# Optimization experiments

Measured on AMD Instinct MI355X. Metric: run time of the kernel, lower is better.

## Reference

```python
import jax, jax.numpy as jnp
import numpy as np

N_NODES = 50000
N_EDGES = 500000
HIDDEN = 128
OUT = 64


def _sage_conv(x, edge_index, Wl, Wr, b):
    # PyG SAGEConv (aggr='mean', root_weight=True):
    # out_i = Wl @ mean_{j->i} x_j + Wr @ x_i + b
    src, dst = edge_index[0], edge_index[1]
    msgs = x[src]                                         # [E, d] gather
    summed = jax.ops.segment_sum(msgs, dst, num_segments=N_NODES)   # [N, d]
    deg = jax.ops.segment_sum(jnp.ones((msgs.shape[0],), x.dtype), dst,
                              num_segments=N_NODES)       # [N]
    agg = summed / jnp.maximum(deg, 1.0)[:, None]         # mean (0 if no in-edges)
    return agg @ Wl + x @ Wr + b


def setup_inputs() -> dict:
    key = jax.random.key(0)
    ks = jax.random.split(key, 11)
    s = 1.0 / np.sqrt(HIDDEN)
    inp = {
        "x": jax.random.normal(ks[0], (N_NODES, HIDDEN), jnp.float32),
        "edge_index": jax.random.randint(ks[1], (2, N_EDGES), 0, N_NODES, jnp.int32),
        "W1l": jax.random.normal(ks[2], (HIDDEN, HIDDEN), jnp.float32) * s,
        "W1r": jax.random.normal(ks[3], (HIDDEN, HIDDEN), jnp.float32) * s,
        "b1": jax.random.normal(ks[4], (HIDDEN,), jnp.float32) * s,
        "W2l": jax.random.normal(ks[5], (HIDDEN, HIDDEN), jnp.float32) * s,
        "W2r": jax.random.normal(ks[6], (HIDDEN, HIDDEN), jnp.float32) * s,
        "b2": jax.random.normal(ks[7], (HIDDEN,), jnp.float32) * s,
        "W3l": jax.random.normal(ks[8], (HIDDEN, OUT), jnp.float32) * s,
        "W3r": jax.random.normal(ks[9], (HIDDEN, OUT), jnp.float32) * s,
        "b3": jax.random.normal(ks[10], (OUT,), jnp.float32) * s,
    }
    return inp


def reference(x, edge_index, W1l, W1r, b1, W2l, W2r, b2, W3l, W3r, b3):
    h = jax.nn.relu(_sage_conv(x, edge_index, W1l, W1r, b1))
    h = jax.nn.relu(_sage_conv(h, edge_index, W2l, W2r, b2))
    return _sage_conv(h, edge_index, W3l, W3r, b3)
```

## Files before the change

### kernel.cpp

```cpp
#include <hip/hip_runtime.h>

typedef unsigned int u32;
typedef unsigned short u16;
typedef __bf16 bf16x8 __attribute__((ext_vector_type(8)));
typedef float f32x4 __attribute__((ext_vector_type(4)));

#define HID 128

__device__ __forceinline__ u16 f2bf(float f) {
  u32 u = __float_as_uint(f);
  u32 r = u + 0x7FFFu + ((u >> 16) & 1u);
  return (u16)(r >> 16);
}
__device__ __forceinline__ float bflo(u32 a) { return __uint_as_float(a << 16); }
__device__ __forceinline__ float bfhi(u32 a) { return __uint_as_float(a & 0xFFFF0000u); }

__global__ void k_deg(const int* __restrict__ dst, int* __restrict__ deg,
                      int* __restrict__ rank, int E) {
  int e = blockIdx.x * blockDim.x + threadIdx.x;
  if (e < E) rank[e] = atomicAdd(&deg[dst[e]], 1);
}

__global__ void k_alloc(const int* __restrict__ deg, int* __restrict__ rp,
                        int* __restrict__ total, int n) {
  int i = blockIdx.x * blockDim.x + threadIdx.x;
  int lane = threadIdx.x & 63;
  int d = (i < n) ? deg[i] : 0;
  int incl = d;
#pragma unroll
  for (int off = 1; off < 64; off <<= 1) {
    int t = __shfl_up(incl, off);
    if (lane >= off) incl += t;
  }
  int wtot = __shfl(incl, 63);
  int base = 0;
  if (lane == 63) base = atomicAdd(total, wtot);
  base = __shfl(base, 63);
  if (i < n) rp[i] = base + incl - d;
}

__global__ void k_scatter(const int* __restrict__ src, const int* __restrict__ dst,
                          const int* __restrict__ rp, const int* __restrict__ rank,
                          int* __restrict__ col, int E) {
  int e = blockIdx.x * blockDim.x + threadIdx.x;
  if (e < E) col[rp[dst[e]] + rank[e]] = src[e];
}

__device__ __forceinline__ void pack_one(const float* __restrict__ W,
                                         u16* __restrict__ P, int N, int t) {
  int lane = t & 63;
  int kt = (t >> 6) & 3;
  int nt = t >> 8;
  int colc = nt * 16 + (lane & 15);
  int krow = kt * 32 + (lane >> 4) * 8;
  u16* d = P + (size_t)t * 8;
#pragma unroll
  for (int j = 0; j < 8; ++j) d[j] = f2bf(W[(krow + j) * N + colc]);
}

__global__ void k_prep(const float* __restrict__ x, u32* __restrict__ xb, int n4,
                       const float* __restrict__ W1l, const float* __restrict__ W1r,
                       const float* __restrict__ W2l, const float* __restrict__ W2r,
                       const float* __restrict__ W3l, const float* __restrict__ W3r,
                       u16* __restrict__ P1l, u16* __restrict__ P1r,
                       u16* __restrict__ P2l, u16* __restrict__ P2r,
                       u16* __restrict__ P3l, u16* __restrict__ P3r) {
  int t = blockIdx.x * blockDim.x + threadIdx.x;
  if (t < 10240) {
    if (t < 2048) pack_one(W1l, P1l, 128, t);
    else if (t < 4096) pack_one(W1r, P1r, 128, t - 2048);
    else if (t < 6144) pack_one(W2l, P2l, 128, t - 4096);
    else if (t < 8192) pack_one(W2r, P2r, 128, t - 6144);
    else if (t < 9216) pack_one(W3l, P3l, 64, t - 8192);
    else pack_one(W3r, P3r, 64, t - 9216);
    return;
  }
  int c = t - 10240;
  if (c < n4) {
    f32x4 v = ((const f32x4*)x)[c];
    u32 o0 = (u32)f2bf(v[0]) | ((u32)f2bf(v[1]) << 16);
    u32 o1 = (u32)f2bf(v[2]) | ((u32)f2bf(v[3]) << 16);
    xb[c * 2] = o0;
    xb[c * 2 + 1] = o1;
  }
}

__global__ void k_agg(const u16* __restrict__ feat, const int* __restrict__ rp,
                      const int* __restrict__ deg, const int* __restrict__ col,
                      u16* __restrict__ agg, int n) {
  int w = (blockIdx.x * blockDim.x + threadIdx.x) >> 6;
  int lane = threadIdx.x & 63;
  if (w >= n) return;
  int beg = rp[w];
  int d = deg[w];
  int end = beg + d;
  const u32* fb = (const u32*)feat + lane;
  float s0 = 0.f, s1 = 0.f, t0 = 0.f, t1 = 0.f;
  float u0 = 0.f, u1 = 0.f, v0 = 0.f, v1 = 0.f;
  int e = beg;
  for (; e + 4 <= end; e += 4) {
    int j0 = col[e], j1 = col[e + 1], j2 = col[e + 2], j3 = col[e + 3];
    u32 a = fb[(size_t)j0 * 64];
    u32 b = fb[(size_t)j1 * 64];
    u32 c = fb[(size_t)j2 * 64];
    u32 dd = fb[(size_t)j3 * 64];
    s0 += bflo(a); s1 += bfhi(a);
    t0 += bflo(b); t1 += bfhi(b);
    u0 += bflo(c); u1 += bfhi(c);
    v0 += bflo(dd); v1 += bfhi(dd);
  }
  for (; e < end; ++e) {
    int j = col[e];
    u32 a = fb[(size_t)j * 64];
    s0 += bflo(a); s1 += bfhi(a);
  }
  float a0 = (s0 + t0) + (u0 + v0);
  float a1 = (s1 + t1) + (u1 + v1);
  float inv = 1.0f / (float)max(d, 1);
  a0 *= inv;
  a1 *= inv;
  *(u32*)(agg + (size_t)w * HID + lane * 2) = (u32)f2bf(a0) | ((u32)f2bf(a1) << 16);
}

template <int NT, int MR, bool RELU, bool OUTF32>
__global__ void k_gemm(const u16* __restrict__ Aagg, const u16* __restrict__ Ah,
                       const u16* __restrict__ Pl, const u16* __restrict__ Pr,
                       const float* __restrict__ bias, void* __restrict__ outp,
                       int mtiles, int n) {
  int wv = (blockIdx.x * blockDim.x + threadIdx.x) >> 6;
  int lane = threadIdx.x & 63;
  int tile0 = wv * MR;
  if (tile0 >= mtiles) return;

  f32x4 acc[MR][NT];
#pragma unroll
  for (int mr = 0; mr < MR; ++mr)
#pragma unroll
    for (int nt = 0; nt < NT; ++nt) acc[mr][nt] = 0.f;

  int rl = lane & 15;
  int kg = lane >> 4;
  int tm[MR];
  const u16 *pa[MR], *ph[MR];
#pragma unroll
  for (int mr = 0; mr < MR; ++mr) {
    tm[mr] = min(tile0 + mr, mtiles - 1);
    int row = tm[mr] * 16 + rl;
    pa[mr] = Aagg + (size_t)row * HID + kg * 8;
    ph[mr] = Ah + (size_t)row * HID + kg * 8;
  }

#pragma unroll
  for (int kt = 0; kt < 4; ++kt) {
    bf16x8 af[MR];
#pragma unroll
    for (int mr = 0; mr < MR; ++mr) af[mr] = *(const bf16x8*)(pa[mr] + kt * 32);
#pragma unroll
    for (int nt = 0; nt < NT; ++nt) {
      bf16x8 bf = *(const bf16x8*)(Pl + ((size_t)(nt * 4 + kt) * 64 + lane) * 8);
#pragma unroll
      for (int mr = 0; mr < MR; ++mr)
        acc[mr][nt] = __builtin_amdgcn_mfma_f32_16x16x32_bf16(af[mr], bf, acc[mr][nt], 0, 0, 0);
    }
  }
#pragma unroll
  for (int kt = 0; kt < 4; ++kt) {
    bf16x8 af[MR];
#pragma unroll
    for (int mr = 0; mr < MR; ++mr) af[mr] = *(const bf16x8*)(ph[mr] + kt * 32);
#pragma unroll
    for (int nt = 0; nt < NT; ++nt) {
      bf16x8 bf = *(const bf16x8*)(Pr + ((size_t)(nt * 4 + kt) * 64 + lane) * 8);
#pragma unroll
      for (int mr = 0; mr < MR; ++mr)
        acc[mr][nt] = __builtin_amdgcn_mfma_f32_16x16x32_bf16(af[mr], bf, acc[mr][nt], 0, 0, 0);
    }
  }

  const int N = NT * 16;
  int rq = lane >> 4;
#pragma unroll
  for (int mr = 0; mr < MR; ++mr) {
#pragma unroll
    for (int nt = 0; nt < NT; ++nt) {
      float bv = bias[nt * 16 + rl];
#pragma unroll
      for (int j = 0; j < 4; ++j) {
        float v = acc[mr][nt][j] + bv;
        if (RELU) v = fmaxf(v, 0.f);
        int r = tm[mr] * 16 + rq * 4 + j;
        if (OUTF32)
          ((float*)outp)[(size_t)r * N + nt * 16 + rl] = v;
        else
          ((u16*)outp)[(size_t)r * N + nt * 16 + rl] = f2bf(v);
      }
    }
  }
}

extern "C" void kernel_launch(void* const* d_in, const int* in_sizes, int n_in,
                              void* d_out, int out_size, void* d_ws, size_t ws_size,
                              hipStream_t stream) {
  const float* x = (const float*)d_in[0];
  const int* ei = (const int*)d_in[1];
  const float* W1l = (const float*)d_in[2];
  const float* W1r = (const float*)d_in[3];
  const float* b1 = (const float*)d_in[4];
  const float* W2l = (const float*)d_in[5];
  const float* W2r = (const float*)d_in[6];
  const float* b2 = (const float*)d_in[7];
  const float* W3l = (const float*)d_in[8];
  const float* W3r = (const float*)d_in[9];
  const float* b3 = (const float*)d_in[10];

  const int E = in_sizes[1] / 2;
  const int N = in_sizes[0] / HID;
  const int* esrc = ei;
  const int* edst = ei + E;

  char* wp = (char*)d_ws;
  auto alloc = [&](size_t b) {
    char* p = wp;
    wp += (b + 255) & ~(size_t)255;
    return p;
  };
  int* deg = (int*)alloc((size_t)(N + 1) * 4);
  int* rp = (int*)alloc((size_t)N * 4);
  int* rank = (int*)alloc((size_t)E * 4);
  int* col = (int*)alloc((size_t)E * 4);
  u16* featA = (u16*)alloc((size_t)N * HID * 2);
  u16* featB = (u16*)alloc((size_t)N * HID * 2);
  u16* aggb = (u16*)alloc((size_t)N * HID * 2);
  u16* P1l = (u16*)alloc(8 * 4 * 64 * 8 * 2);
  u16* P1r = (u16*)alloc(8 * 4 * 64 * 8 * 2);
  u16* P2l = (u16*)alloc(8 * 4 * 64 * 8 * 2);
  u16* P2r = (u16*)alloc(8 * 4 * 64 * 8 * 2);
  u16* P3l = (u16*)alloc(4 * 4 * 64 * 8 * 2);
  u16* P3r = (u16*)alloc(4 * 4 * 64 * 8 * 2);

  hipMemsetAsync(deg, 0, (size_t)(N + 1) * 4, stream);

  int eb = (E + 255) / 256;
  k_deg<<<eb, 256, 0, stream>>>(edst, deg, rank, E);
  k_alloc<<<(N + 255) / 256, 256, 0, stream>>>(deg, rp, deg + N, N);
  k_scatter<<<eb, 256, 0, stream>>>(esrc, edst, rp, rank, col, E);

  int n4 = N * (HID / 4);
  k_prep<<<(10240 + n4 + 255) / 256, 256, 0, stream>>>(
      x, (u32*)featA, n4, W1l, W1r, W2l, W2r, W3l, W3r, P1l, P1r, P2l, P2r, P3l, P3r);

  int ab = (N * 64 + 255) / 256;
  int mtiles = N / 16;
  int gwaves = (mtiles + 1) / 2;
  int gb = (gwaves * 64 + 255) / 256;

  k_agg<<<ab, 256, 0, stream>>>(featA, rp, deg, col, aggb, N);
  k_gemm<8, 2, true, false><<<gb, 256, 0, stream>>>(aggb, featA, P1l, P1r, b1, featB, mtiles, N);
  k_agg<<<ab, 256, 0, stream>>>(featB, rp, deg, col, aggb, N);
  k_gemm<8, 2, true, false><<<gb, 256, 0, stream>>>(aggb, featB, P2l, P2r, b2, featA, mtiles, N);
  k_agg<<<ab, 256, 0, stream>>>(featA, rp, deg, col, aggb, N);
  k_gemm<4, 2, false, true><<<gb, 256, 0, stream>>>(aggb, featA, P3l, P3r, b3, (float*)d_out, mtiles, N);
}
```

Baseline: 273.5 us.

## Fuse mean aggregation and dual GEMM into one per-layer kernel via LDS

Replaces the separate aggregation and GEMM kernels with a single per-layer kernel. Each wave gathers and averages neighbor features for 16 nodes, writes them to shared memory, and feeds them straight into MFMA alongside the root features. This removes the global aggregation buffer round-trip and three kernel launches. In exchange, each wave now processes 16 nodes serially, so far fewer waves are available to hide the latency of the irregular gathers.

```diff
diff --git a/kernel.cpp b/kernel.cpp
--- a/kernel.cpp
+++ b/kernel.cpp
@@ -78,122 +78,99 @@
   int c = t - 10240;
   if (c < n4) {
     f32x4 v = ((const f32x4*)x)[c];
-    u32 o0 = (u32)f2bf(v[0]) | ((u32)f2bf(v[1]) << 16);
-    u32 o1 = (u32)f2bf(v[2]) | ((u32)f2bf(v[3]) << 16);
-    xb[c * 2] = o0;
-    xb[c * 2 + 1] = o1;
-  }
-}
-
-__global__ void k_agg(const u16* __restrict__ feat, const int* __restrict__ rp,
-                      const int* __restrict__ deg, const int* __restrict__ col,
-                      u16* __restrict__ agg, int n) {
-  int w = (blockIdx.x * blockDim.x + threadIdx.x) >> 6;
+    xb[c * 2] = (u32)f2bf(v[0]) | ((u32)f2bf(v[1]) << 16);
+    xb[c * 2 + 1] = (u32)f2bf(v[2]) | ((u32)f2bf(v[3]) << 16);
+  }
+}
+
+template <int NT, bool RELU, bool OUTF32>
+__global__ void k_layer(const u16* __restrict__ feat, const int* __restrict__ rp,
+                        const int* __restrict__ deg, const int* __restrict__ col,
+                        const u16* __restrict__ Pl, const u16* __restrict__ Pr,
+                        const float* __restrict__ bias, void* __restrict__ outp,
+                        int n) {
+  __shared__ u32 sm[4][16][68];
+  int wave = threadIdx.x >> 6;
   int lane = threadIdx.x & 63;
-  if (w >= n) return;
-  int beg = rp[w];
-  int d = deg[w];
-  int end = beg + d;
+  int g0 = blockIdx.x * 64 + wave * 16;
+  if (g0 >= n) return;
+
   const u32* fb = (const u32*)feat + lane;
-  float s0 = 0.f, s1 = 0.f, t0 = 0.f, t1 = 0.f;
-  float u0 = 0.f, u1 = 0.f, v0 = 0.f, v1 = 0.f;
-  int e = beg;
-  for (; e + 4 <= end; e += 4) {
-    int j0 = col[e], j1 = col[e + 1], j2 = col[e + 2], j3 = col[e + 3];
-    u32 a = fb[(size_t)j0 * 64];
-    u32 b = fb[(size_t)j1 * 64];
-    u32 c = fb[(size_t)j2 * 64];
-    u32 dd = fb[(size_t)j3 * 64];
-    s0 += bflo(a); s1 += bfhi(a);
-    t0 += bflo(b); t1 += bfhi(b);
-    u0 += bflo(c); u1 += bfhi(c);
-    v0 += bflo(dd); v1 += bfhi(dd);
-  }
-  for (; e < end; ++e) {
-    int j = col[e];
-    u32 a = fb[(size_t)j * 64];
-    s0 += bflo(a); s1 += bfhi(a);
-  }
-  float a0 = (s0 + t0) + (u0 + v0);
-  float a1 = (s1 + t1) + (u1 + v1);
-  float inv = 1.0f / (float)max(d, 1);
-  a0 *= inv;
-  a1 *= inv;
-  *(u32*)(agg + (size_t)w * HID + lane * 2) = (u32)f2bf(a0) | ((u32)f2bf(a1) << 16);
-}
-
-template <int NT, int MR, bool RELU, bool OUTF32>
-__global__ void k_gemm(const u16* __restrict__ Aagg, const u16* __restrict__ Ah,
-                       const u16* __restrict__ Pl, const u16* __restrict__ Pr,
-                       const float* __restrict__ bias, void* __restrict__ outp,
-                       int mtiles, int n) {
-  int wv = (blockIdx.x * blockDim.x + threadIdx.x) >> 6;
-  int lane = threadIdx.x & 63;
-  int tile0 = wv * MR;
-  if (tile0 >= mtiles) return;
-
-  f32x4 acc[MR][NT];
-#pragma unroll
-  for (int mr = 0; mr < MR; ++mr)
-#pragma unroll
-    for (int nt = 0; nt < NT; ++nt) acc[mr][nt] = 0.f;
+  for (int r = 0; r < 16; ++r) {
+    int g = g0 + r;
+    if (g >= n) break;
+    int beg = rp[g];
+    int d = deg[g];
+    int end = beg + d;
+    float s0 = 0.f, s1 = 0.f, t0 = 0.f, t1 = 0.f;
+    float u0 = 0.f, u1 = 0.f, v0 = 0.f, v1 = 0.f;
+    int e = beg;
+    for (; e + 4 <= end; e += 4) {
+      int j0 = col[e], j1 = col[e + 1], j2 = col[e + 2], j3 = col[e + 3];
+      u32 a = fb[(size_t)j0 * 64];
+      u32 b = fb[(size_t)j1 * 64];
+      u32 c = fb[(size_t)j2 * 64];
+      u32 dd = fb[(size_t)j3 * 64];
+      s0 += bflo(a); s1 += bfhi(a);
+      t0 += bflo(b); t1 += bfhi(b);
+      u0 += bflo(c); u1 += bfhi(c);
+      v0 += bflo(dd); v1 += bfhi(dd);
+    }
+    for (; e < end; ++e) {
+      u32 a = fb[(size_t)col[e] * 64];
+      s0 += bflo(a); s1 += bfhi(a);
+    }
+    float a0 = (s0 + t0) + (u0 + v0);
+    float a1 = (s1 + t1) + (u1 + v1);
+    float inv = 1.0f / (float)max(d, 1);
+    a0 *= inv;
+    a1 *= inv;
+    sm[wave][r][lane] = (u32)f2bf(a0) | ((u32)f2bf(a1) << 16);
+  }
 
   int rl = lane & 15;
   int kg = lane >> 4;
-  int tm[MR];
-  const u16 *pa[MR], *ph[MR];
-#pragma unroll
-  for (int mr = 0; mr < MR; ++mr) {
-    tm[mr] = min(tile0 + mr, mtiles - 1);
-    int row = tm[mr] * 16 + rl;
-    pa[mr] = Aagg + (size_t)row * HID + kg * 8;
-    ph[mr] = Ah + (size_t)row * HID + kg * 8;
-  }
+  f32x4 acc[NT];
+#pragma unroll
+  for (int nt = 0; nt < NT; ++nt) acc[nt] = 0.f;
+
+  int grow = min(g0 + rl, n - 1);
+  const u16* ph = feat + (size_t)grow * HID + kg * 8;
 
 #pragma unroll
   for (int kt = 0; kt < 4; ++kt) {
-    bf16x8 af[MR];
-#pragma unroll
-    for (int mr = 0; mr < MR; ++mr) af[mr] = *(const bf16x8*)(pa[mr] + kt * 32);
+    bf16x8 aa = *(const bf16x8*)&sm[wave][rl][kt * 16 + kg * 4];
 #pragma unroll
     for (int nt = 0; nt < NT; ++nt) {
       bf16x8 bf = *(const bf16x8*)(Pl + ((size_t)(nt * 4 + kt) * 64 + lane) * 8);
-#pragma unroll
-      for (int mr = 0; mr < MR; ++mr)
-        acc[mr][nt] = __builtin_amdgcn_mfma_f32_16x16x32_bf16(af[mr], bf, acc[mr][nt], 0, 0, 0);
+      acc[nt] = __builtin_amdgcn_mfma_f32_16x16x32_bf16(aa, bf, acc[nt], 0, 0, 0);
     }
   }
 #pragma unroll
   for (int kt = 0; kt < 4; ++kt) {
-    bf16x8 af[MR];
-#pragma unroll
-    for (int mr = 0; mr < MR; ++mr) af[mr] = *(const bf16x8*)(ph[mr] + kt * 32);
+    bf16x8 ah = *(const bf16x8*)(ph + kt * 32);
 #pragma unroll
     for (int nt = 0; nt < NT; ++nt) {
       bf16x8 bf = *(const bf16x8*)(Pr + ((size_t)(nt * 4 + kt) * 64 + lane) * 8);
-#pragma unroll
-      for (int mr = 0; mr < MR; ++mr)
-        acc[mr][nt] = __builtin_amdgcn_mfma_f32_16x16x32_bf16(af[mr], bf, acc[mr][nt], 0, 0, 0);
+      acc[nt] = __builtin_amdgcn_mfma_f32_16x16x32_bf16(ah, bf, acc[nt], 0, 0, 0);
     }
   }
 
   const int N = NT * 16;
   int rq = lane >> 4;
 #pragma unroll
-  for (int mr = 0; mr < MR; ++mr) {
-#pragma unroll
-    for (int nt = 0; nt < NT; ++nt) {
-      float bv = bias[nt * 16 + rl];
-#pragma unroll
-      for (int j = 0; j < 4; ++j) {
-        float v = acc[mr][nt][j] + bv;
-        if (RELU) v = fmaxf(v, 0.f);
-        int r = tm[mr] * 16 + rq * 4 + j;
-        if (OUTF32)
-          ((float*)outp)[(size_t)r * N + nt * 16 + rl] = v;
-        else
-          ((u16*)outp)[(size_t)r * N + nt * 16 + rl] = f2bf(v);
-      }
+  for (int nt = 0; nt < NT; ++nt) {
+    float bv = bias[nt * 16 + rl];
+#pragma unroll
+    for (int j = 0; j < 4; ++j) {
+      int r = g0 + rq * 4 + j;
+      if (r >= n) continue;
+      float v = acc[nt][j] + bv;
+      if (RELU) v = fmaxf(v, 0.f);
+      if (OUTF32)
+        ((float*)outp)[(size_t)r * N + nt * 16 + rl] = v;
+      else
+        ((u16*)outp)[(size_t)r * N + nt * 16 + rl] = f2bf(v);
     }
   }
 }
@@ -230,7 +207,6 @@
   int* col = (int*)alloc((size_t)E * 4);
   u16* featA = (u16*)alloc((size_t)N * HID * 2);
   u16* featB = (u16*)alloc((size_t)N * HID * 2);
-  u16* aggb = (u16*)alloc((size_t)N * HID * 2);
   u16* P1l = (u16*)alloc(8 * 4 * 64 * 8 * 2);
   u16* P1r = (u16*)alloc(8 * 4 * 64 * 8 * 2);
   u16* P2l = (u16*)alloc(8 * 4 * 64 * 8 * 2);
@@ -249,15 +225,9 @@
   k_prep<<<(10240 + n4 + 255) / 256, 256, 0, stream>>>(
       x, (u32*)featA, n4, W1l, W1r, W2l, W2r, W3l, W3r, P1l, P1r, P2l, P2r, P3l, P3r);
 
-  int ab = (N * 64 + 255) / 256;
-  int mtiles = N / 16;
-  int gwaves = (mtiles + 1) / 2;
-  int gb = (gwaves * 64 + 255) / 256;
-
-  k_agg<<<ab, 256, 0, stream>>>(featA, rp, deg, col, aggb, N);
-  k_gemm<8, 2, true, false><<<gb, 256, 0, stream>>>(aggb, featA, P1l, P1r, b1, featB, mtiles, N);
-  k_agg<<<ab, 256, 0, stream>>>(featB, rp, deg, col, aggb, N);
-  k_gemm<8, 2, true, false><<<gb, 256, 0, stream>>>(aggb, featB, P2l, P2r, b2, featA, mtiles, N);
-  k_agg<<<ab, 256, 0, stream>>>(featA, rp, deg, col, aggb, N);
-  k_gemm<4, 2, false, true><<<gb, 256, 0, stream>>>(aggb, featA, P3l, P3r, b3, (float*)d_out, mtiles, N);
-}
+  int lb = (N + 63) / 64;
+
+  k_layer<8, true, false><<<lb, 256, 0, stream>>>(featA, rp, deg, col, P1l, P1r, b1, featB, N);
+  k_layer<8, true, false><<<lb, 256, 0, stream>>>(featB, rp, deg, col, P2l, P2r, b2, featA, N);
+  k_layer<4, false, true><<<lb, 256, 0, stream>>>(featA, rp, deg, col, P3l, P3r, b3, (float*)d_out, N);
+}
```

Result: slower. 323.8 us (+18.4%).
